# Optimization experiments

Hardware: AMD Instinct MI355X
Metric: run time of the kernel (lower is better)

## Reference

```python
import jax, jax.numpy as jnp
import numpy as np

N = 50000      # nodes
E_RAND = 600000  # random edges per meta-path
M = 3          # meta-paths
D_IN = 128
D_OUT = 128
H_SEM = 128    # SemanticAttention hidden (default 128)
NEG_SLOPE = 0.2  # DGL GATConv leaky_relu default


def setup_inputs() -> dict:
    key = jax.random.key(0)
    ks = jax.random.split(key, 12)
    h = jax.random.normal(ks[0], (N, D_IN), dtype=jnp.float32)
    src = jax.random.randint(ks[1], (M, E_RAND), 0, N, dtype=jnp.int32)
    dst = jax.random.randint(ks[2], (M, E_RAND), 0, N, dtype=jnp.int32)
    # add self-loops (dgl.add_self_loop): guarantees every dst has >=1 edge
    loops = jnp.broadcast_to(jnp.arange(N, dtype=jnp.int32), (M, N))
    edge_src = jnp.concatenate([src, loops], axis=1)
    edge_dst = jnp.concatenate([dst, loops], axis=1)
    W_gat = jax.random.normal(ks[3], (M, D_IN, D_OUT), dtype=jnp.float32) * 0.05
    attn_l = jax.random.normal(ks[4], (M, D_OUT), dtype=jnp.float32) * 0.1
    attn_r = jax.random.normal(ks[5], (M, D_OUT), dtype=jnp.float32) * 0.1
    bias_gat = jax.random.normal(ks[6], (M, D_OUT), dtype=jnp.float32) * 0.02
    Ws1 = jax.random.normal(ks[7], (D_OUT, H_SEM), dtype=jnp.float32) * 0.05
    bs1 = jnp.zeros((H_SEM,), dtype=jnp.float32)
    Ws2 = jax.random.normal(ks[8], (H_SEM,), dtype=jnp.float32) * 0.05
    return {"h": h, "edge_src": edge_src, "edge_dst": edge_dst,
            "W_gat": W_gat, "attn_l": attn_l, "attn_r": attn_r,
            "bias_gat": bias_gat, "Ws1": Ws1, "bs1": bs1, "Ws2": Ws2}


def _gat_meta_path(feat_m, el_m, er_m, src, dst):
    # feat_m: [N, D]; el/er: [N]; src/dst: [E]
    e = jax.nn.leaky_relu(el_m[src] + er_m[dst], NEG_SLOPE)  # [E]
    emax = jax.ops.segment_max(e, dst, num_segments=N)       # [N]
    ex = jnp.exp(e - emax[dst])
    denom = jax.ops.segment_sum(ex, dst, num_segments=N)     # [N]
    a = ex / denom[dst]                                      # edge softmax
    # scatter-aggregate weighted source features -> [N, D]
    return jax.ops.segment_sum(a[:, None] * feat_m[src], dst, num_segments=N)


def reference(h, edge_src, edge_dst, W_gat, attn_l, attn_r, bias_gat, Ws1, bs1, Ws2):
    # per-meta-path GATConv projections
    feat = jnp.einsum('ni,mio->mno', h, W_gat)            # [M, N, D]
    el = jnp.einsum('mno,mo->mn', feat, attn_l)           # [M, N]
    er = jnp.einsum('mno,mo->mn', feat, attn_r)           # [M, N]
    z = jax.vmap(_gat_meta_path)(feat, el, er, edge_src, edge_dst)  # [M, N, D]
    z = jax.nn.elu(z + bias_gat[:, None, :])              # GATConv bias + activation
    z = jnp.transpose(z, (1, 0, 2))                       # [N, M, D]
    # SemanticAttention: Linear -> tanh -> Linear(no bias), mean over nodes, softmax over meta-paths
    w = jnp.einsum('nmh,h->nm', jnp.tanh(jnp.einsum('nmd,dh->nmh', z, Ws1) + bs1), Ws2)
    beta = jax.nn.softmax(w.mean(0))                      # [M]
    return jnp.einsum('m,nmd->nd', beta, z)               # [N, D]
```

## Files before the change

### kernel.cpp

```cpp
#include <hip/hip_runtime.h>
#include <hip/hip_fp16.h>

#define NV 50000
#define EE 650000
#define MM 3
#define NBUK 196
#define PADCAP 2048
#define CSRSTRIDE (EE + NBUK * PADCAP)
#define CHSZ 4096
#define NCH 159
#define SEMBLK 586

typedef __attribute__((ext_vector_type(8))) __bf16 bf16x8;
typedef __attribute__((ext_vector_type(8))) _Float16 f16x8;
typedef __attribute__((ext_vector_type(8))) unsigned short u16x8;
typedef __attribute__((ext_vector_type(4))) float f32x4;

__device__ __forceinline__ unsigned short f2bf(float f) {
    unsigned u = __builtin_bit_cast(unsigned, f);
    u += 0x7FFFu + ((u >> 16) & 1u);
    return (unsigned short)(u >> 16);
}
__device__ __forceinline__ bf16x8 zero8() {
    u16x8 u = {0,0,0,0,0,0,0,0};
    return __builtin_bit_cast(bf16x8, u);
}
__device__ __forceinline__ f16x8 zero8h() {
    u16x8 u = {0,0,0,0,0,0,0,0};
    return __builtin_bit_cast(f16x8, u);
}
__device__ __forceinline__ unsigned short f2h(float f) {
    return __builtin_bit_cast(unsigned short, __float2half(f));
}

__global__ void prep_all(const float* __restrict__ h, const float* __restrict__ Wg,
                         const float* __restrict__ Ws1, unsigned* __restrict__ hb,
                         unsigned short* __restrict__ WT, unsigned short* __restrict__ WsT) {
    int idx = blockIdx.x * 256 + threadIdx.x;
    if (idx < NV * 64) {
        float2 f = *reinterpret_cast<const float2*>(h + (size_t)idx * 2);
        hb[idx] = ((unsigned)f2bf(f.x)) | (((unsigned)f2bf(f.y)) << 16);
    } else if (idx < NV * 64 + MM * 16384) {
        int r0 = idx - NV * 64;
        int m = r0 / 16384, r = r0 % 16384;
        int o = r >> 7, d = r & 127;
        WT[r0] = f2bf(Wg[m * 16384 + d * 128 + o]);
    } else {
        int r = idx - NV * 64 - MM * 16384;
        int j = r >> 7, d = r & 127;
        WsT[r] = f2h(Ws1[d * 128 + j]);
    }
}

__global__ __launch_bounds__(256, 2) void gemm_feat(
    const unsigned short* __restrict__ hb, const unsigned short* __restrict__ WT,
    const float* __restrict__ attn_l, const float* __restrict__ attn_r,
    unsigned* __restrict__ featb, float* __restrict__ el, float* __restrict__ er) {
    const int m = blockIdx.y;
    const int tid = threadIdx.x;
    const int wave = tid >> 6, lane = tid & 63;
    const int lo = lane & 15, hi = lane >> 4;
    const int rowbase = blockIdx.x * 256 + wave * 64;
    const unsigned short* WTm = WT + m * 16384;

    f32x4 acc[4][8];
#pragma unroll
    for (int a = 0; a < 4; ++a)
#pragma unroll
        for (int b = 0; b < 8; ++b) acc[a][b] = (f32x4){0.f, 0.f, 0.f, 0.f};

#pragma unroll
    for (int kk = 0; kk < 4; ++kk) {
        bf16x8 bfrag[8];
#pragma unroll
        for (int ct = 0; ct < 8; ++ct)
            bfrag[ct] = *reinterpret_cast<const bf16x8*>(WTm + (ct * 16 + lo) * 128 + kk * 32 + hi * 8);
#pragma unroll
        for (int rt = 0; rt < 4; ++rt) {
            int row = rowbase + rt * 16 + lo;
            bf16x8 af = (row < NV)
                ? *reinterpret_cast<const bf16x8*>(hb + (size_t)row * 128 + kk * 32 + hi * 8)
                : zero8();
#pragma unroll
            for (int ct = 0; ct < 8; ++ct)
                acc[rt][ct] = __builtin_amdgcn_mfma_f32_16x16x32_bf16(af, bfrag[ct], acc[rt][ct], 0, 0, 0);
        }
    }

    float alv[8], arv[8];
#pragma unroll
    for (int ct = 0; ct < 8; ++ct) {
        alv[ct] = attn_l[m * 128 + ct * 16 + lo];
        arv[ct] = attn_r[m * 128 + ct * 16 + lo];
    }

#pragma unroll
    for (int rt = 0; rt < 4; ++rt) {
        float pl[4] = {0.f, 0.f, 0.f, 0.f}, pr[4] = {0.f, 0.f, 0.f, 0.f};
#pragma unroll
        for (int ct = 0; ct < 8; ++ct)
#pragma unroll
            for (int i = 0; i < 4; ++i) {
                pl[i] += acc[rt][ct][i] * alv[ct];
                pr[i] += acc[rt][ct][i] * arv[ct];
            }
#pragma unroll
        for (int s = 1; s < 16; s <<= 1)
#pragma unroll
            for (int i = 0; i < 4; ++i) {
                pl[i] += __shfl_xor(pl[i], s, 64);
                pr[i] += __shfl_xor(pr[i], s, 64);
            }
        int row0 = rowbase + rt * 16 + hi * 4;
        if (lo == 0) {
#pragma unroll
            for (int i = 0; i < 4; ++i)
                if (row0 + i < NV) {
                    el[m * NV + row0 + i] = pl[i];
                    er[m * NV + row0 + i] = pr[i];
                }
        }
#pragma unroll
        for (int ct = 0; ct < 8; ++ct)
#pragma unroll
            for (int i = 0; i < 4; ++i) {
                float v = acc[rt][ct][i];
                float vp = __shfl_xor(v, 1, 64);
                int row = row0 + i;
                if (((lo & 1) == 0) && row < NV) {
                    unsigned pk = ((unsigned)f2h(v)) | (((unsigned)f2h(vp)) << 16);
                    featb[(size_t)(m * NV + row) * 64 + ct * 8 + (lo >> 1)] = pk;
                }
            }
    }
}

__global__ __launch_bounds__(256) void hist_k(const int* __restrict__ edst,
                                              int* __restrict__ counts) {
    int m = blockIdx.y, c = blockIdx.x, tid = threadIdx.x;
    __shared__ int hsm[NBUK];
    if (tid < NBUK) hsm[tid] = 0;
    __syncthreads();
    int base = c * CHSZ;
#pragma unroll
    for (int i = 0; i < CHSZ / 256; ++i) {
        int e = base + i * 256 + tid;
        if (e < EE) {
            int d = edst[(size_t)m * EE + e];
            atomicAdd(&hsm[d >> 8], 1);
        }
    }
    __syncthreads();
    if (tid < NBUK) counts[(m * NCH + c) * NBUK + tid] = hsm[tid];
}

__global__ __launch_bounds__(256) void scanP1_k(const int* __restrict__ counts,
                                                int* __restrict__ chunkpos,
                                                int* __restrict__ btot) {
    int b = blockIdx.x, m = blockIdx.y, t = threadIdx.x;
    __shared__ int sm[256];
    int v = (t < NCH) ? counts[(m * NCH + t) * NBUK + b] : 0;
    sm[t] = v;
    __syncthreads();
#pragma unroll
    for (int s = 1; s < 256; s <<= 1) {
        int add = (t >= s) ? sm[t - s] : 0;
        __syncthreads();
        sm[t] += add;
        __syncthreads();
    }
    if (t < NCH) chunkpos[(m * NCH + t) * NBUK + b] = sm[t] - v;
    if (t == 0) btot[m * NBUK + b] = sm[255];
}

__global__ __launch_bounds__(256) void scanP2_k(const int* __restrict__ btot,
                                                int* __restrict__ bstart) {
    int m = blockIdx.x, t = threadIdx.x;
    __shared__ int sm[256];
    int v = (t < NBUK) ? btot[m * NBUK + t] : 0;
    sm[t] = v;
    __syncthreads();
#pragma unroll
    for (int s = 1; s < 256; s <<= 1) {
        int add = (t >= s) ? sm[t - s] : 0;
        __syncthreads();
        sm[t] += add;
        __syncthreads();
    }
    if (t < NBUK) bstart[m * NBUK + t] = sm[t] - v;
}

__global__ __launch_bounds__(256) void scat1_k(const int* __restrict__ esrc,
                                               const int* __restrict__ edst,
                                               const int* __restrict__ chunkpos,
                                               const int* __restrict__ bstart,
                                               unsigned* __restrict__ staging) {
    int m = blockIdx.y, c = blockIdx.x, tid = threadIdx.x;
    __shared__ int cnt[NBUK];
    __shared__ int sofs[NBUK];
    if (tid < NBUK) {
        cnt[tid] = 0;
        sofs[tid] = bstart[m * NBUK + tid] + chunkpos[(m * NCH + c) * NBUK + tid];
    }
    __syncthreads();
    int base = c * CHSZ;
#pragma unroll
    for (int i = 0; i < CHSZ / 256; ++i) {
        int e = base + i * 256 + tid;
        if (e < EE) {
            int s = esrc[(size_t)m * EE + e];
            int d = edst[(size_t)m * EE + e];
            int b = d >> 8;
            int r = atomicAdd(&cnt[b], 1);
            staging[(size_t)m * EE + sofs[b] + r] =
                ((unsigned)(d & 255) << 16) | (unsigned)s;
        }
    }
}

__global__ __launch_bounds__(256) void bsort_k(const unsigned* __restrict__ staging,
                                               const int* __restrict__ bstart,
                                               const float* __restrict__ el,
                                               const float* __restrict__ er,
                                               unsigned* __restrict__ csr,
                                               int* __restrict__ start,
                                               int* __restrict__ deg,
                                               float* __restrict__ dinv) {
    int b = blockIdx.x, m = blockIdx.y, t = threadIdx.x;
    __shared__ int hsm[256];
    __shared__ int sc[256];
    __shared__ int cur[256];
    __shared__ float dsum[256];
    hsm[t] = 0;
    dsum[t] = 0.f;
    __syncthreads();
    int sbase = bstart[m * NBUK + b];
    int nseg = ((b == NBUK - 1) ? EE : bstart[m * NBUK + b + 1]) - sbase;
    const unsigned* sp = staging + (size_t)m * EE + sbase;
    for (int i = t; i < nseg; i += 256)
        atomicAdd(&hsm[sp[i] >> 16], 1);
    __syncthreads();
    int v = hsm[t];
    int pv = (v + 7) & ~7;
    sc[t] = pv;
    __syncthreads();
#pragma unroll
    for (int s = 1; s < 256; s <<= 1) {
        int add = (t >= s) ? sc[t - s] : 0;
        __syncthreads();
        sc[t] += add;
        __syncthreads();
    }
    int pexcl = sc[t] - pv;
    int pb = ((sbase + 7) & ~7) + b * PADCAP;
    cur[t] = pb + pexcl;
    int node = (b << 8) + t;
    if (node < NV) {
        deg[m * NV + node] = pv;
        start[m * NV + node] = pb + pexcl;
    }
    unsigned* cpm = csr + (size_t)m * CSRSTRIDE;
    for (int k = v; k < pv; ++k) cpm[pb + pexcl + k] = 0;
    __syncthreads();
    int node0 = b << 8;
    for (int i = t; i < nseg; i += 256) {
        unsigned rec = sp[i];
        int dloc = rec >> 16;
        int s = rec & 0xFFFF;
        float x = el[m * NV + s] + er[m * NV + node0 + dloc];
        x = x > 0.f ? x : 0.2f * x;
        float ex = __expf(x);
        atomicAdd(&dsum[dloc], ex);
        int slot = atomicAdd(&cur[dloc], 1);
        cpm[slot] = ((unsigned)f2h(ex) << 16) | (unsigned)s;
    }
    __syncthreads();
    if (node < NV) dinv[m * NV + node] = 1.f / dsum[t];
}

__global__ __launch_bounds__(256, 4) void aggregate_k(
    const unsigned* __restrict__ featb, const unsigned* __restrict__ csr,
    const int* __restrict__ start, const int* __restrict__ deg,
    const float* __restrict__ dinv, const float* __restrict__ bias,
    unsigned* __restrict__ zh) {
    int wid = blockIdx.x * 4 + (threadIdx.x >> 6);
    int gw = wid * 2 + ((threadIdx.x >> 5) & 1);
    int sl = threadIdx.x & 31;
    int m = gw / NV;
    int st = start[gw];
    int dg = deg[gw];
    const unsigned* pp = csr + (size_t)m * CSRSTRIDE + st;
    const unsigned* fb = featb + (size_t)m * NV * 64 + sl * 2;
    float a0 = 0.f, a1 = 0.f, a2 = 0.f, a3 = 0.f;
    for (int e0 = 0; e0 < dg; e0 += 8) {
        uint4 r0 = *reinterpret_cast<const uint4*>(pp + e0);
        uint4 r1 = *reinterpret_cast<const uint4*>(pp + e0 + 4);
        unsigned p[8] = {r0.x, r0.y, r0.z, r0.w, r1.x, r1.y, r1.z, r1.w};
        uint2 v[8];
#pragma unroll
        for (int i = 0; i < 8; ++i) {
            unsigned off = (p[i] & 0xFFFFu) << 6;
            v[i] = *reinterpret_cast<const uint2*>(fb + off);
        }
#pragma unroll
        for (int i = 0; i < 8; ++i) {
            float x = __half2float(__builtin_bit_cast(__half, (unsigned short)(p[i] >> 16)));
            __half2 h0 = __builtin_bit_cast(__half2, v[i].x);
            __half2 h1 = __builtin_bit_cast(__half2, v[i].y);
            a0 = fmaf(x, __low2float(h0),  a0);
            a1 = fmaf(x, __high2float(h0), a1);
            a2 = fmaf(x, __low2float(h1),  a2);
            a3 = fmaf(x, __high2float(h1), a3);
        }
    }
    float inv = dinv[gw];
    int d0 = sl * 4;
    const float* bp = bias + m * 128 + d0;
    float z0 = a0 * inv + bp[0];
    float z1 = a1 * inv + bp[1];
    float z2 = a2 * inv + bp[2];
    float z3 = a3 * inv + bp[3];
    z0 = z0 > 0.f ? z0 : (__expf(z0) - 1.f);
    z1 = z1 > 0.f ? z1 : (__expf(z1) - 1.f);
    z2 = z2 > 0.f ? z2 : (__expf(z2) - 1.f);
    z3 = z3 > 0.f ? z3 : (__expf(z3) - 1.f);
    uint2 o;
    o.x = ((unsigned)f2h(z0)) | (((unsigned)f2h(z1)) << 16);
    o.y = ((unsigned)f2h(z2)) | (((unsigned)f2h(z3)) << 16);
    *reinterpret_cast<uint2*>(zh + (size_t)gw * 64 + sl * 2) = o;
}

__global__ __launch_bounds__(256, 2) void semantic_k(
    const unsigned* __restrict__ zh, const unsigned short* __restrict__ WsT,
    const float* __restrict__ bs1, const float* __restrict__ Ws2,
    float* __restrict__ wpart) {
    const int tid = threadIdx.x;
    const int wave = tid >> 6, lane = tid & 63;
    const int lo = lane & 15, hi = lane >> 4;
    const int rowbase = blockIdx.x * 256 + wave * 64;

    f32x4 acc[4][8];
#pragma unroll
    for (int a = 0; a < 4; ++a)
#pragma unroll
        for (int b = 0; b < 8; ++b) acc[a][b] = (f32x4){0.f, 0.f, 0.f, 0.f};

#pragma unroll
    for (int kk = 0; kk < 4; ++kk) {
        f16x8 bfrag[8];
#pragma unroll
        for (int ct = 0; ct < 8; ++ct)
            bfrag[ct] = *reinterpret_cast<const f16x8*>(WsT + (ct * 16 + lo) * 128 + kk * 32 + hi * 8);
#pragma unroll
        for (int rt = 0; rt < 4; ++rt) {
            int row = rowbase + rt * 16 + lo;
            f16x8 af = (row < MM * NV)
                ? *reinterpret_cast<const f16x8*>(zh + (size_t)row * 64 + kk * 16 + hi * 2)
                : zero8h();
#pragma unroll
            for (int ct = 0; ct < 8; ++ct)
                acc[rt][ct] = __builtin_amdgcn_mfma_f32_16x16x32_f16(af, bfrag[ct], acc[rt][ct], 0, 0, 0);
        }
    }

    float w2v[8], b1v[8];
#pragma unroll
    for (int ct = 0; ct < 8; ++ct) {
        w2v[ct] = Ws2[ct * 16 + lo];
        b1v[ct] = bs1[ct * 16 + lo];
    }

    float t0 = 0.f, t1 = 0.f, t2 = 0.f;
#pragma unroll
    for (int rt = 0; rt < 4; ++rt) {
        int rbase = rowbase + rt * 16;
        if (rbase >= MM * NV) continue;
        int mm = rbase / NV;
        float p = 0.f;
#pragma unroll
        for (int ct = 0; ct < 8; ++ct)
#pragma unroll
            for (int i = 0; i < 4; ++i) {
                float x = acc[rt][ct][i] + b1v[ct];
                x = fminf(fmaxf(x, -15.f), 15.f);
                float t = __expf(2.f * x);
                p += w2v[ct] * ((t - 1.f) / (t + 1.f));
            }
#pragma unroll
        for (int s = 1; s < 64; s <<= 1) p += __shfl_xor(p, s, 64);
        if (mm == 0) t0 += p; else if (mm == 1) t1 += p; else t2 += p;
    }

    __shared__ float smw[4][3];
    if (lane == 0) { smw[wave][0] = t0; smw[wave][1] = t1; smw[wave][2] = t2; }
    __syncthreads();
    if (tid < 3)
        wpart[blockIdx.x * 4 + tid] =
            smw[0][tid] + smw[1][tid] + smw[2][tid] + smw[3][tid];
}

__global__ __launch_bounds__(64) void beta_k(const float* __restrict__ wpart,
                                             float* __restrict__ beta) {
    int lane = threadIdx.x;
    float t0 = 0.f, t1 = 0.f, t2 = 0.f;
    for (int b = lane; b < SEMBLK; b += 64) {
        t0 += wpart[b * 4 + 0];
        t1 += wpart[b * 4 + 1];
        t2 += wpart[b * 4 + 2];
    }
#pragma unroll
    for (int s = 1; s < 64; s <<= 1) {
        t0 += __shfl_xor(t0, s, 64);
        t1 += __shfl_xor(t1, s, 64);
        t2 += __shfl_xor(t2, s, 64);
    }
    if (lane == 0) {
        float w0 = t0 * (1.f / NV), w1 = t1 * (1.f / NV), w2 = t2 * (1.f / NV);
        float mx = fmaxf(w0, fmaxf(w1, w2));
        float e0 = __expf(w0 - mx), e1 = __expf(w1 - mx), e2 = __expf(w2 - mx);
        float inv = 1.f / (e0 + e1 + e2);
        beta[0] = e0 * inv; beta[1] = e1 * inv; beta[2] = e2 * inv;
    }
}

__global__ __launch_bounds__(256) void combine_k(const unsigned* __restrict__ zh,
                                                 const float* __restrict__ beta,
                                                 float* __restrict__ out) {
    int idx = blockIdx.x * 256 + threadIdx.x;
    float b0 = beta[0], b1 = beta[1], b2 = beta[2];
    uint2 u0 = *reinterpret_cast<const uint2*>(zh + (size_t)idx * 2);
    uint2 u1 = *reinterpret_cast<const uint2*>(zh + (size_t)NV * 64 + (size_t)idx * 2);
    uint2 u2 = *reinterpret_cast<const uint2*>(zh + (size_t)2 * NV * 64 + (size_t)idx * 2);
    float2 a0 = __half22float2(__builtin_bit_cast(__half2, u0.x));
    float2 a1 = __half22float2(__builtin_bit_cast(__half2, u0.y));
    float2 c0 = __half22float2(__builtin_bit_cast(__half2, u1.x));
    float2 c1 = __half22float2(__builtin_bit_cast(__half2, u1.y));
    float2 d0 = __half22float2(__builtin_bit_cast(__half2, u2.x));
    float2 d1 = __half22float2(__builtin_bit_cast(__half2, u2.y));
    float4 o;
    o.x = b0 * a0.x + b1 * c0.x + b2 * d0.x;
    o.y = b0 * a0.y + b1 * c0.y + b2 * d0.y;
    o.z = b0 * a1.x + b1 * c1.x + b2 * d1.x;
    o.w = b0 * a1.y + b1 * c1.y + b2 * d1.y;
    *reinterpret_cast<float4*>(out + (size_t)idx * 4) = o;
}

extern "C" void kernel_launch(void* const* d_in, const int* in_sizes, int n_in,
                              void* d_out, int out_size, void* d_ws, size_t ws_size,
                              hipStream_t stream) {
    const float* h      = (const float*)d_in[0];
    const int*   esrc   = (const int*)d_in[1];
    const int*   edst   = (const int*)d_in[2];
    const float* Wg     = (const float*)d_in[3];
    const float* attn_l = (const float*)d_in[4];
    const float* attn_r = (const float*)d_in[5];
    const float* bias   = (const float*)d_in[6];
    const float* Ws1    = (const float*)d_in[7];
    const float* bs1    = (const float*)d_in[8];
    const float* Ws2    = (const float*)d_in[9];
    float* out = (float*)d_out;

    char* w = (char*)d_ws;
    auto alloc = [&](size_t bytes) { char* p = w; w += (bytes + 255) & ~(size_t)255; return p; };
    unsigned short* WT   = (unsigned short*)alloc((size_t)MM * 128 * 128 * 2);
    unsigned short* WsT  = (unsigned short*)alloc((size_t)128 * 128 * 2);
    unsigned* hb    = (unsigned*)alloc((size_t)NV * 64 * 4);
    unsigned* featb = (unsigned*)alloc((size_t)MM * NV * 64 * 4);
    unsigned* zh    = (unsigned*)alloc((size_t)MM * NV * 64 * 4);
    float* el     = (float*)alloc((size_t)MM * NV * 4);
    float* er     = (float*)alloc((size_t)MM * NV * 4);
    float* dinv   = (float*)alloc((size_t)MM * NV * 4);
    int*   deg    = (int*)alloc((size_t)MM * NV * 4);
    int*   startb = (int*)alloc((size_t)MM * NV * 4);
    int*   counts = (int*)alloc((size_t)MM * NCH * NBUK * 4);
    int*   chunkpos = (int*)alloc((size_t)MM * NCH * NBUK * 4);
    int*   btot   = (int*)alloc((size_t)MM * NBUK * 4);
    int*   bstart = (int*)alloc((size_t)MM * NBUK * 4);
    unsigned* staging = (unsigned*)alloc((size_t)MM * EE * 4);
    unsigned* csr     = (unsigned*)alloc((size_t)MM * CSRSTRIDE * 4);
    float* wpart  = (float*)alloc((size_t)SEMBLK * 4 * 4);
    float* beta   = (float*)alloc(256);

    hipLaunchKernelGGL(prep_all, dim3((NV * 64 + (MM + 1) * 16384) / 256), dim3(256), 0, stream,
                       h, Wg, Ws1, hb, WT, WsT);
    hipLaunchKernelGGL(gemm_feat, dim3(196, MM), dim3(256), 0, stream,
                       (const unsigned short*)hb, WT, attn_l, attn_r, featb, el, er);
    hipLaunchKernelGGL(hist_k, dim3(NCH, MM), dim3(256), 0, stream, edst, counts);
    hipLaunchKernelGGL(scanP1_k, dim3(NBUK, MM), dim3(256), 0, stream, counts, chunkpos, btot);
    hipLaunchKernelGGL(scanP2_k, dim3(MM), dim3(256), 0, stream, btot, bstart);
    hipLaunchKernelGGL(scat1_k, dim3(NCH, MM), dim3(256), 0, stream,
                       esrc, edst, chunkpos, bstart, staging);
    hipLaunchKernelGGL(bsort_k, dim3(NBUK, MM), dim3(256), 0, stream,
                       staging, bstart, el, er, csr, startb, deg, dinv);
    hipLaunchKernelGGL(aggregate_k, dim3((MM * NV) / 8), dim3(256), 0, stream,
                       featb, csr, startb, deg, dinv, bias, zh);
    hipLaunchKernelGGL(semantic_k, dim3(SEMBLK), dim3(256), 0, stream,
                       zh, WsT, bs1, Ws2, wpart);
    hipLaunchKernelGGL(beta_k, dim3(1), dim3(64), 0, stream, wpart, beta);
    hipLaunchKernelGGL(combine_k, dim3(6250), dim3(256), 0, stream, zh, beta, out);
}
```

Baseline: 213.3 us.

## Merge independent kernels into shared launches and fold beta into combine

Packs the prep conversion and the edge histogram into one launch, and the feature GEMM and edge scatter into another, each using block-index ranges so independent work runs side by side. The beta softmax kernel is folded into combine, where every block redundantly reduces wpart and then grid-strides over the output. The semantic kernel's occupancy hint rises from 2 to 3 blocks. This cuts launch count and per-kernel tail idle time, at the cost of mixed-resource blocks sharing one register and LDS budget and repeated small reductions in combine.

```diff
diff --git a/kernel.cpp b/kernel.cpp
--- a/kernel.cpp
+++ b/kernel.cpp
@@ -10,6 +10,7 @@
 #define CHSZ 4096
 #define NCH 159
 #define SEMBLK 586
+#define PREPBLK 12756
 
 typedef __attribute__((ext_vector_type(8))) __bf16 bf16x8;
 typedef __attribute__((ext_vector_type(8))) _Float16 f16x8;
@@ -33,125 +34,44 @@
     return __builtin_bit_cast(unsigned short, __float2half(f));
 }
 
-__global__ void prep_all(const float* __restrict__ h, const float* __restrict__ Wg,
-                         const float* __restrict__ Ws1, unsigned* __restrict__ hb,
-                         unsigned short* __restrict__ WT, unsigned short* __restrict__ WsT) {
-    int idx = blockIdx.x * 256 + threadIdx.x;
-    if (idx < NV * 64) {
-        float2 f = *reinterpret_cast<const float2*>(h + (size_t)idx * 2);
-        hb[idx] = ((unsigned)f2bf(f.x)) | (((unsigned)f2bf(f.y)) << 16);
-    } else if (idx < NV * 64 + MM * 16384) {
-        int r0 = idx - NV * 64;
-        int m = r0 / 16384, r = r0 % 16384;
-        int o = r >> 7, d = r & 127;
-        WT[r0] = f2bf(Wg[m * 16384 + d * 128 + o]);
+__global__ void prep_hist(const float* __restrict__ h, const float* __restrict__ Wg,
+                          const float* __restrict__ Ws1, const int* __restrict__ edst,
+                          unsigned* __restrict__ hb, unsigned short* __restrict__ WT,
+                          unsigned short* __restrict__ WsT, int* __restrict__ counts) {
+    if (blockIdx.x < PREPBLK) {
+        int idx = blockIdx.x * 256 + threadIdx.x;
+        if (idx < NV * 64) {
+            float2 f = *reinterpret_cast<const float2*>(h + (size_t)idx * 2);
+            hb[idx] = ((unsigned)f2bf(f.x)) | (((unsigned)f2bf(f.y)) << 16);
+        } else if (idx < NV * 64 + MM * 16384) {
+            int r0 = idx - NV * 64;
+            int m = r0 / 16384, r = r0 % 16384;
+            int o = r >> 7, d = r & 127;
+            WT[r0] = f2bf(Wg[m * 16384 + d * 128 + o]);
+        } else {
+            int r = idx - NV * 64 - MM * 16384;
+            int j = r >> 7, d = r & 127;
+            WsT[r] = f2h(Ws1[d * 128 + j]);
+        }
     } else {
-        int r = idx - NV * 64 - MM * 16384;
-        int j = r >> 7, d = r & 127;
-        WsT[r] = f2h(Ws1[d * 128 + j]);
-    }
-}
-
-__global__ __launch_bounds__(256, 2) void gemm_feat(
-    const unsigned short* __restrict__ hb, const unsigned short* __restrict__ WT,
-    const float* __restrict__ attn_l, const float* __restrict__ attn_r,
-    unsigned* __restrict__ featb, float* __restrict__ el, float* __restrict__ er) {
-    const int m = blockIdx.y;
-    const int tid = threadIdx.x;
-    const int wave = tid >> 6, lane = tid & 63;
-    const int lo = lane & 15, hi = lane >> 4;
-    const int rowbase = blockIdx.x * 256 + wave * 64;
-    const unsigned short* WTm = WT + m * 16384;
-
-    f32x4 acc[4][8];
-#pragma unroll
-    for (int a = 0; a < 4; ++a)
-#pragma unroll
-        for (int b = 0; b < 8; ++b) acc[a][b] = (f32x4){0.f, 0.f, 0.f, 0.f};
-
-#pragma unroll
-    for (int kk = 0; kk < 4; ++kk) {
-        bf16x8 bfrag[8];
-#pragma unroll
-        for (int ct = 0; ct < 8; ++ct)
-            bfrag[ct] = *reinterpret_cast<const bf16x8*>(WTm + (ct * 16 + lo) * 128 + kk * 32 + hi * 8);
-#pragma unroll
-        for (int rt = 0; rt < 4; ++rt) {
-            int row = rowbase + rt * 16 + lo;
-            bf16x8 af = (row < NV)
-                ? *reinterpret_cast<const bf16x8*>(hb + (size_t)row * 128 + kk * 32 + hi * 8)
-                : zero8();
-#pragma unroll
-            for (int ct = 0; ct < 8; ++ct)
-                acc[rt][ct] = __builtin_amdgcn_mfma_f32_16x16x32_bf16(af, bfrag[ct], acc[rt][ct], 0, 0, 0);
-        }
-    }
-
-    float alv[8], arv[8];
-#pragma unroll
-    for (int ct = 0; ct < 8; ++ct) {
-        alv[ct] = attn_l[m * 128 + ct * 16 + lo];
-        arv[ct] = attn_r[m * 128 + ct * 16 + lo];
-    }
-
-#pragma unroll
-    for (int rt = 0; rt < 4; ++rt) {
-        float pl[4] = {0.f, 0.f, 0.f, 0.f}, pr[4] = {0.f, 0.f, 0.f, 0.f};
-#pragma unroll
-        for (int ct = 0; ct < 8; ++ct)
-#pragma unroll
-            for (int i = 0; i < 4; ++i) {
-                pl[i] += acc[rt][ct][i] * alv[ct];
-                pr[i] += acc[rt][ct][i] * arv[ct];
+        int bi = blockIdx.x - PREPBLK;
+        int m = bi / NCH, c = bi % NCH;
+        int tid = threadIdx.x;
+        __shared__ int hsm[NBUK];
+        if (tid < NBUK) hsm[tid] = 0;
+        __syncthreads();
+        int base = c * CHSZ;
+#pragma unroll
+        for (int i = 0; i < CHSZ / 256; ++i) {
+            int e = base + i * 256 + tid;
+            if (e < EE) {
+                int d = edst[(size_t)m * EE + e];
+                atomicAdd(&hsm[d >> 8], 1);
             }
-#pragma unroll
-        for (int s = 1; s < 16; s <<= 1)
-#pragma unroll
-            for (int i = 0; i < 4; ++i) {
-                pl[i] += __shfl_xor(pl[i], s, 64);
-                pr[i] += __shfl_xor(pr[i], s, 64);
-            }
-        int row0 = rowbase + rt * 16 + hi * 4;
-        if (lo == 0) {
-#pragma unroll
-            for (int i = 0; i < 4; ++i)
-                if (row0 + i < NV) {
-                    el[m * NV + row0 + i] = pl[i];
-                    er[m * NV + row0 + i] = pr[i];
-                }
-        }
-#pragma unroll
-        for (int ct = 0; ct < 8; ++ct)
-#pragma unroll
-            for (int i = 0; i < 4; ++i) {
-                float v = acc[rt][ct][i];
-                float vp = __shfl_xor(v, 1, 64);
-                int row = row0 + i;
-                if (((lo & 1) == 0) && row < NV) {
-                    unsigned pk = ((unsigned)f2h(v)) | (((unsigned)f2h(vp)) << 16);
-                    featb[(size_t)(m * NV + row) * 64 + ct * 8 + (lo >> 1)] = pk;
-                }
-            }
-    }
-}
-
-__global__ __launch_bounds__(256) void hist_k(const int* __restrict__ edst,
-                                              int* __restrict__ counts) {
-    int m = blockIdx.y, c = blockIdx.x, tid = threadIdx.x;
-    __shared__ int hsm[NBUK];
-    if (tid < NBUK) hsm[tid] = 0;
-    __syncthreads();
-    int base = c * CHSZ;
-#pragma unroll
-    for (int i = 0; i < CHSZ / 256; ++i) {
-        int e = base + i * 256 + tid;
-        if (e < EE) {
-            int d = edst[(size_t)m * EE + e];
-            atomicAdd(&hsm[d >> 8], 1);
-        }
-    }
-    __syncthreads();
-    if (tid < NBUK) counts[(m * NCH + c) * NBUK + tid] = hsm[tid];
+        }
+        __syncthreads();
+        if (tid < NBUK) counts[(m * NCH + c) * NBUK + tid] = hsm[tid];
+    }
 }
 
 __global__ __launch_bounds__(256) void scanP1_k(const int* __restrict__ counts,
@@ -190,30 +110,115 @@
     if (t < NBUK) bstart[m * NBUK + t] = sm[t] - v;
 }
 
-__global__ __launch_bounds__(256) void scat1_k(const int* __restrict__ esrc,
-                                               const int* __restrict__ edst,
-                                               const int* __restrict__ chunkpos,
-                                               const int* __restrict__ bstart,
-                                               unsigned* __restrict__ staging) {
-    int m = blockIdx.y, c = blockIdx.x, tid = threadIdx.x;
-    __shared__ int cnt[NBUK];
-    __shared__ int sofs[NBUK];
-    if (tid < NBUK) {
-        cnt[tid] = 0;
-        sofs[tid] = bstart[m * NBUK + tid] + chunkpos[(m * NCH + c) * NBUK + tid];
-    }
-    __syncthreads();
-    int base = c * CHSZ;
-#pragma unroll
-    for (int i = 0; i < CHSZ / 256; ++i) {
-        int e = base + i * 256 + tid;
-        if (e < EE) {
-            int s = esrc[(size_t)m * EE + e];
-            int d = edst[(size_t)m * EE + e];
-            int b = d >> 8;
-            int r = atomicAdd(&cnt[b], 1);
-            staging[(size_t)m * EE + sofs[b] + r] =
-                ((unsigned)(d & 255) << 16) | (unsigned)s;
+__global__ __launch_bounds__(256, 2) void gemm_scat(
+    const unsigned short* __restrict__ hb, const unsigned short* __restrict__ WT,
+    const float* __restrict__ attn_l, const float* __restrict__ attn_r,
+    unsigned* __restrict__ featb, float* __restrict__ el, float* __restrict__ er,
+    const int* __restrict__ esrc, const int* __restrict__ edst,
+    const int* __restrict__ chunkpos, const int* __restrict__ bstart,
+    unsigned* __restrict__ staging) {
+    if (blockIdx.x < 196 * MM) {
+        const int m = blockIdx.x / 196;
+        const int bx = blockIdx.x % 196;
+        const int tid = threadIdx.x;
+        const int wave = tid >> 6, lane = tid & 63;
+        const int lo = lane & 15, hi = lane >> 4;
+        const int rowbase = bx * 256 + wave * 64;
+        const unsigned short* WTm = WT + m * 16384;
+
+        f32x4 acc[4][8];
+#pragma unroll
+        for (int a = 0; a < 4; ++a)
+#pragma unroll
+            for (int b = 0; b < 8; ++b) acc[a][b] = (f32x4){0.f, 0.f, 0.f, 0.f};
+
+#pragma unroll
+        for (int kk = 0; kk < 4; ++kk) {
+            bf16x8 bfrag[8];
+#pragma unroll
+            for (int ct = 0; ct < 8; ++ct)
+                bfrag[ct] = *reinterpret_cast<const bf16x8*>(WTm + (ct * 16 + lo) * 128 + kk * 32 + hi * 8);
+#pragma unroll
+            for (int rt = 0; rt < 4; ++rt) {
+                int row = rowbase + rt * 16 + lo;
+                bf16x8 af = (row < NV)
+                    ? *reinterpret_cast<const bf16x8*>(hb + (size_t)row * 128 + kk * 32 + hi * 8)
+                    : zero8();
+#pragma unroll
+                for (int ct = 0; ct < 8; ++ct)
+                    acc[rt][ct] = __builtin_amdgcn_mfma_f32_16x16x32_bf16(af, bfrag[ct], acc[rt][ct], 0, 0, 0);
+            }
+        }
+
+        float alv[8], arv[8];
+#pragma unroll
+        for (int ct = 0; ct < 8; ++ct) {
+            alv[ct] = attn_l[m * 128 + ct * 16 + lo];
+            arv[ct] = attn_r[m * 128 + ct * 16 + lo];
+        }
+
+#pragma unroll
+        for (int rt = 0; rt < 4; ++rt) {
+            float pl[4] = {0.f, 0.f, 0.f, 0.f}, pr[4] = {0.f, 0.f, 0.f, 0.f};
+#pragma unroll
+            for (int ct = 0; ct < 8; ++ct)
+#pragma unroll
+                for (int i = 0; i < 4; ++i) {
+                    pl[i] += acc[rt][ct][i] * alv[ct];
+                    pr[i] += acc[rt][ct][i] * arv[ct];
+                }
+#pragma unroll
+            for (int s = 1; s < 16; s <<= 1)
+#pragma unroll
+                for (int i = 0; i < 4; ++i) {
+                    pl[i] += __shfl_xor(pl[i], s, 64);
+                    pr[i] += __shfl_xor(pr[i], s, 64);
+                }
+            int row0 = rowbase + rt * 16 + hi * 4;
+            if (lo == 0) {
+#pragma unroll
+                for (int i = 0; i < 4; ++i)
+                    if (row0 + i < NV) {
+                        el[m * NV + row0 + i] = pl[i];
+                        er[m * NV + row0 + i] = pr[i];
+                    }
+            }
+#pragma unroll
+            for (int ct = 0; ct < 8; ++ct)
+#pragma unroll
+                for (int i = 0; i < 4; ++i) {
+                    float v = acc[rt][ct][i];
+                    float vp = __shfl_xor(v, 1, 64);
+                    int row = row0 + i;
+                    if (((lo & 1) == 0) && row < NV) {
+                        unsigned pk = ((unsigned)f2h(v)) | (((unsigned)f2h(vp)) << 16);
+                        featb[(size_t)(m * NV + row) * 64 + ct * 8 + (lo >> 1)] = pk;
+                    }
+                }
+        }
+    } else {
+        int bi = blockIdx.x - 196 * MM;
+        int m = bi / NCH, c = bi % NCH;
+        int tid = threadIdx.x;
+        __shared__ int cnt[NBUK];
+        __shared__ int sofs[NBUK];
+        if (tid < NBUK) {
+            cnt[tid] = 0;
+            sofs[tid] = bstart[m * NBUK + tid] + chunkpos[(m * NCH + c) * NBUK + tid];
+        }
+        __syncthreads();
+        int base = c * CHSZ;
+#pragma unroll
+        for (int i = 0; i < CHSZ / 256; ++i) {
+            int e = base + i * 256 + tid;
+            if (e < EE) {
+                int s = esrc[(size_t)m * EE + e];
+                int d = edst[(size_t)m * EE + e];
+                int b = d >> 8;
+                int r = atomicAdd(&cnt[b], 1);
+                staging[(size_t)m * EE + sofs[b] + r] =
+                    ((unsigned)(d & 255) << 16) | (unsigned)s;
+            }
         }
     }
 }
@@ -330,7 +335,7 @@
     *reinterpret_cast<uint2*>(zh + (size_t)gw * 64 + sl * 2) = o;
 }
 
-__global__ __launch_bounds__(256, 2) void semantic_k(
+__global__ __launch_bounds__(256, 3) void semantic_k(
     const unsigned* __restrict__ zh, const unsigned short* __restrict__ WsT,
     const float* __restrict__ bs1, const float* __restrict__ Ws2,
     float* __restrict__ wpart) {
@@ -399,11 +404,12 @@
             smw[0][tid] + smw[1][tid] + smw[2][tid] + smw[3][tid];
 }
 
-__global__ __launch_bounds__(64) void beta_k(const float* __restrict__ wpart,
-                                             float* __restrict__ beta) {
-    int lane = threadIdx.x;
+__global__ __launch_bounds__(256) void combine_k(const unsigned* __restrict__ zh,
+                                                 const float* __restrict__ wpart,
+                                                 float* __restrict__ out) {
+    int tid = threadIdx.x, lane = tid & 63, wv = tid >> 6;
     float t0 = 0.f, t1 = 0.f, t2 = 0.f;
-    for (int b = lane; b < SEMBLK; b += 64) {
+    for (int b = tid; b < SEMBLK; b += 256) {
         t0 += wpart[b * 4 + 0];
         t1 += wpart[b * 4 + 1];
         t2 += wpart[b * 4 + 2];
@@ -414,35 +420,34 @@
         t1 += __shfl_xor(t1, s, 64);
         t2 += __shfl_xor(t2, s, 64);
     }
-    if (lane == 0) {
-        float w0 = t0 * (1.f / NV), w1 = t1 * (1.f / NV), w2 = t2 * (1.f / NV);
-        float mx = fmaxf(w0, fmaxf(w1, w2));
-        float e0 = __expf(w0 - mx), e1 = __expf(w1 - mx), e2 = __expf(w2 - mx);
-        float inv = 1.f / (e0 + e1 + e2);
-        beta[0] = e0 * inv; beta[1] = e1 * inv; beta[2] = e2 * inv;
-    }
-}
-
-__global__ __launch_bounds__(256) void combine_k(const unsigned* __restrict__ zh,
-                                                 const float* __restrict__ beta,
-                                                 float* __restrict__ out) {
-    int idx = blockIdx.x * 256 + threadIdx.x;
-    float b0 = beta[0], b1 = beta[1], b2 = beta[2];
-    uint2 u0 = *reinterpret_cast<const uint2*>(zh + (size_t)idx * 2);
-    uint2 u1 = *reinterpret_cast<const uint2*>(zh + (size_t)NV * 64 + (size_t)idx * 2);
-    uint2 u2 = *reinterpret_cast<const uint2*>(zh + (size_t)2 * NV * 64 + (size_t)idx * 2);
-    float2 a0 = __half22float2(__builtin_bit_cast(__half2, u0.x));
-    float2 a1 = __half22float2(__builtin_bit_cast(__half2, u0.y));
-    float2 c0 = __half22float2(__builtin_bit_cast(__half2, u1.x));
-    float2 c1 = __half22float2(__builtin_bit_cast(__half2, u1.y));
-    float2 d0 = __half22float2(__builtin_bit_cast(__half2, u2.x));
-    float2 d1 = __half22float2(__builtin_bit_cast(__half2, u2.y));
-    float4 o;
-    o.x = b0 * a0.x + b1 * c0.x + b2 * d0.x;
-    o.y = b0 * a0.y + b1 * c0.y + b2 * d0.y;
-    o.z = b0 * a1.x + b1 * c1.x + b2 * d1.x;
-    o.w = b0 * a1.y + b1 * c1.y + b2 * d1.y;
-    *reinterpret_cast<float4*>(out + (size_t)idx * 4) = o;
+    __shared__ float sb[4][3];
+    if (lane == 0) { sb[wv][0] = t0; sb[wv][1] = t1; sb[wv][2] = t2; }
+    __syncthreads();
+    float w0 = (sb[0][0] + sb[1][0] + sb[2][0] + sb[3][0]) * (1.f / NV);
+    float w1 = (sb[0][1] + sb[1][1] + sb[2][1] + sb[3][1]) * (1.f / NV);
+    float w2 = (sb[0][2] + sb[1][2] + sb[2][2] + sb[3][2]) * (1.f / NV);
+    float mx = fmaxf(w0, fmaxf(w1, w2));
+    float e0 = __expf(w0 - mx), e1 = __expf(w1 - mx), e2 = __expf(w2 - mx);
+    float inv = 1.f / (e0 + e1 + e2);
+    float b0 = e0 * inv, b1 = e1 * inv, b2 = e2 * inv;
+
+    for (int idx = blockIdx.x * 256 + tid; idx < NV * 32; idx += SEMBLK * 256) {
+        uint2 u0 = *reinterpret_cast<const uint2*>(zh + (size_t)idx * 2);
+        uint2 u1 = *reinterpret_cast<const uint2*>(zh + (size_t)NV * 64 + (size_t)idx * 2);
+        uint2 u2 = *reinterpret_cast<const uint2*>(zh + (size_t)2 * NV * 64 + (size_t)idx * 2);
+        float2 a0 = __half22float2(__builtin_bit_cast(__half2, u0.x));
+        float2 a1 = __half22float2(__builtin_bit_cast(__half2, u0.y));
+        float2 c0 = __half22float2(__builtin_bit_cast(__half2, u1.x));
+        float2 c1 = __half22float2(__builtin_bit_cast(__half2, u1.y));
+        float2 d0 = __half22float2(__builtin_bit_cast(__half2, u2.x));
+        float2 d1 = __half22float2(__builtin_bit_cast(__half2, u2.y));
+        float4 o;
+        o.x = b0 * a0.x + b1 * c0.x + b2 * d0.x;
+        o.y = b0 * a0.y + b1 * c0.y + b2 * d0.y;
+        o.z = b0 * a1.x + b1 * c1.x + b2 * d1.x;
+        o.w = b0 * a1.y + b1 * c1.y + b2 * d1.y;
+        *reinterpret_cast<float4*>(out + (size_t)idx * 4) = o;
+    }
 }
 
 extern "C" void kernel_launch(void* const* d_in, const int* in_sizes, int n_in,
@@ -479,16 +484,13 @@
     unsigned* staging = (unsigned*)alloc((size_t)MM * EE * 4);
     unsigned* csr     = (unsigned*)alloc((size_t)MM * CSRSTRIDE * 4);
     float* wpart  = (float*)alloc((size_t)SEMBLK * 4 * 4);
-    float* beta   = (float*)alloc(256);
-
-    hipLaunchKernelGGL(prep_all, dim3((NV * 64 + (MM + 1) * 16384) / 256), dim3(256), 0, stream,
-                       h, Wg, Ws1, hb, WT, WsT);
-    hipLaunchKernelGGL(gemm_feat, dim3(196, MM), dim3(256), 0, stream,
-                       (const unsigned short*)hb, WT, attn_l, attn_r, featb, el, er);
-    hipLaunchKernelGGL(hist_k, dim3(NCH, MM), dim3(256), 0, stream, edst, counts);
+
+    hipLaunchKernelGGL(prep_hist, dim3(PREPBLK + MM * NCH), dim3(256), 0, stream,
+                       h, Wg, Ws1, edst, hb, WT, WsT, counts);
     hipLaunchKernelGGL(scanP1_k, dim3(NBUK, MM), dim3(256), 0, stream, counts, chunkpos, btot);
     hipLaunchKernelGGL(scanP2_k, dim3(MM), dim3(256), 0, stream, btot, bstart);
-    hipLaunchKernelGGL(scat1_k, dim3(NCH, MM), dim3(256), 0, stream,
+    hipLaunchKernelGGL(gemm_scat, dim3(196 * MM + MM * NCH), dim3(256), 0, stream,
+                       (const unsigned short*)hb, WT, attn_l, attn_r, featb, el, er,
                        esrc, edst, chunkpos, bstart, staging);
     hipLaunchKernelGGL(bsort_k, dim3(NBUK, MM), dim3(256), 0, stream,
                        staging, bstart, el, er, csr, startb, deg, dinv);
@@ -496,6 +498,5 @@
                        featb, csr, startb, deg, dinv, bias, zh);
     hipLaunchKernelGGL(semantic_k, dim3(SEMBLK), dim3(256), 0, stream,
                        zh, WsT, bs1, Ws2, wpart);
-    hipLaunchKernelGGL(beta_k, dim3(1), dim3(64), 0, stream, wpart, beta);
-    hipLaunchKernelGGL(combine_k, dim3(6250), dim3(256), 0, stream, zh, beta, out);
-}
+    hipLaunchKernelGGL(combine_k, dim3(SEMBLK), dim3(256), 0, stream, zh, wpart, out);
+}
```

Measured after the change: 232.6 us. 9.0% more time.
